# Optimization experiments

Measured on AMD Instinct MI355X. Metric: run time of the kernel, lower is better.

The kernel has to match this reference:

```python
import jax, jax.numpy as jnp
import numpy as np
from jax import lax

B, HCH, NCODES, H, W = 16, 32, 256, 256, 256

def conv2d(x, w, b, pad):
    y = lax.conv_general_dilated(x, w, (1, 1), [(pad, pad), (pad, pad)],
                                 dimension_numbers=('NCHW', 'OIHW', 'NCHW'))
    return y + b[None, :, None, None]

def vq(z, codebook):
    # z: (B,C,H,W); codebook: (K,C)
    zf = jnp.transpose(z, (0, 2, 3, 1)).reshape(-1, z.shape[1])  # (BHW,C)
    dists = (zf ** 2).sum(1, keepdims=True) + (codebook ** 2).sum(1) - 2.0 * zf @ codebook.T
    idx = jnp.argmin(dists, axis=1)
    zq = codebook[idx].reshape(z.shape[0], z.shape[2], z.shape[3], z.shape[1])
    zq = jnp.transpose(zq, (0, 3, 1, 2))
    # straight-through estimator
    return z + lax.stop_gradient(zq - z)

def setup_inputs() -> dict:
    key = jax.random.key(0)
    ks = jax.random.split(key, 12)
    s = lambda k, shp, scale=0.1: (jax.random.normal(k, shp, jnp.float32) * scale)
    return {
        'x': jax.random.normal(ks[0], (B, 1, H, W), jnp.float32),
        'stem_w': s(ks[1], (HCH, 1, 3, 3)),
        'stem_b': s(ks[2], (HCH,)),
        'up1_w': s(ks[3], (HCH, HCH, 3, 3)),
        'up1_b': s(ks[4], (HCH,)),
        'up2_w': s(ks[5], (HCH, HCH, 1, 1)),
        'up2_b': s(ks[6], (HCH,)),
        'tau_w': s(ks[7], (HCH, HCH, 1, 1)),
        'tau_b': s(ks[8], (HCH,)),
        'codebook': jax.random.uniform(ks[9], (NCODES, HCH), jnp.float32,
                                       -1.0 / NCODES, 1.0 / NCODES),
        'dec_w': s(ks[10], (1, HCH, 1, 1)),
        'dec_b': s(ks[11], (1,)),
        'n_steps': 5,
    }

def reference(x, stem_w, stem_b, up1_w, up1_b, up2_w, up2_b, tau_w, tau_b,
              codebook, dec_w, dec_b, n_steps):
    state = jax.nn.relu(conv2d(x, stem_w, stem_b, 1))
    for t in range(n_steps):
        delta = conv2d(jax.nn.relu(conv2d(state, up1_w, up1_b, 1)), up2_w, up2_b, 0)
        beta = jax.nn.sigmoid(conv2d(state, tau_w, tau_b, 0))
        state = beta * state + (1.0 - beta) * delta
        state = vq(state, codebook)  # vq_every = 1
    return jax.nn.sigmoid(conv2d(state, dec_w, dec_b, 0))
```

## Files before the change

### kernel.cpp

```cpp
#include <hip/hip_runtime.h>
#include <hip/hip_bf16.h>

#define BATCH 16
#define HH 256
#define WW 256
#define NPIX (BATCH*HH*WW)
#define NSTEPS 5
#define CBS 40

#define W1F 0
#define W2F 9216
#define WTF 10240
#define CBF 11264
#define IDF 19456
#define W1P 20480
#define W2P 29696
#define WTP 30720
#define IDP 31744
#define CBP 32768
#define FRAGS_TOT 40960

using u16 = unsigned short;
using u32 = unsigned int;
using u8  = unsigned char;

typedef __attribute__((ext_vector_type(8))) short bf8_t;
typedef __attribute__((ext_vector_type(4))) float f4_t;

#define MFMA16 __builtin_amdgcn_mfma_f32_16x16x32_bf16

#define DPPMIN(v, CTRL) do { \
    u32 _o = (u32)__builtin_amdgcn_update_dpp((int)(v), (int)(v), (CTRL), 0xF, 0xF, false); \
    (v) = _o < (v) ? _o : (v); } while (0)

#define LDS_ORDER() asm volatile("" ::: "memory")

__device__ __forceinline__ float bf2f(u32 u) {
    union { u32 i; float f; } v; v.i = u << 16; return v.f;
}
__device__ __forceinline__ u16 f2bf(float f) {
    union { float f; u32 i; } v; v.f = f;
    u32 x = v.i;
    x += 0x7fffu + ((x >> 16) & 1u);
    return (u16)(x >> 16);
}
__device__ __forceinline__ u32 pack2bf(float a, float b) {
    __hip_bfloat162 h2 = __float22bfloat162_rn(float2{a, b});
    union { __hip_bfloat162 h; u32 u; } v; v.h = h2; return v.u;
}
__device__ __forceinline__ float ldin(const void* p, int i, int f32) {
    return f32 ? ((const float*)p)[i] : bf2f(((const u16*)p)[i]);
}
__device__ __forceinline__ u16 ldbf(const void* p, int i, int f32) {
    return f32 ? f2bf(((const float*)p)[i]) : ((const u16*)p)[i];
}
__device__ __forceinline__ int sniff_f32(const void* xraw) {
    const u32* xw = (const u32*)xraw;
    int cnt = 0;
    for (int j = 0; j < 64; j++) {
        u32 w = xw[j];
        float flo = bf2f(w & 0xffffu);
        float a = fabsf(flo);
        if (flo == 0.0f || (a >= 6e-8f && a <= 64.0f)) cnt++;
    }
    return (cnt < 32) ? 1 : 0;
}
__device__ __forceinline__ int chperm(int kp) { return (kp >> 1) | ((kp & 1) << 4); }

__global__ void prep_kernel(const void* x,
    const void* stem_w, const void* stem_b, const void* up1_w, const void* up1_b,
    const void* up2_w, const void* up2_b, const void* tau_w, const void* tau_b,
    const void* cb, const void* dec_w, const void* dec_b,
    u16* frags, u16* cb_bf,
    float* cn2, float* cadj, float* decdot, float* wf0,
    float* up1_bf, float* up2_bf, float* tau_bf, float* stem_bf, int* flag)
{
    int f32 = sniff_f32(x);
    int i = blockIdx.x * 256 + threadIdx.x;
    if (i == 0) *flag = f32;
    if (i < 9216) {
        int slot = i >> 9, rem = i & 511, lane = rem >> 3, j = rem & 7;
        int tap = slot >> 1, nt = slot & 1;
        int co = nt*16 + (lane & 15), ci = (lane >> 4)*8 + j;
        frags[W1F + i] = ldbf(up1_w, (co*32+ci)*9 + tap, f32);
        return;
    }
    i -= 9216;
    if (i < 1024) {
        int nt = i >> 9, rem = i & 511, lane = rem >> 3, j = rem & 7;
        int co = nt*16 + (lane & 15), k = (lane >> 4)*8 + j;
        frags[W2F + i] = ldbf(up2_w, co*32 + k, f32);
        return;
    }
    i -= 1024;
    if (i < 1024) {
        int nt = i >> 9, rem = i & 511, lane = rem >> 3, j = rem & 7;
        int co = nt*16 + (lane & 15), k = (lane >> 4)*8 + j;
        frags[WTF + i] = ldbf(tau_w, co*32 + k, f32);
        return;
    }
    i -= 1024;
    if (i < 8192) {
        int nt = i >> 9, rem = i & 511, lane = rem >> 3, j = rem & 7;
        int code = nt*16 + (lane & 15), c = (lane >> 4)*8 + j;
        frags[CBF + i] = ldbf(cb, code*32 + c, f32);
        return;
    }
    i -= 8192;
    if (i < 1024) {
        int s = i >> 9, rem = i & 511, lane = rem >> 3, j = rem & 7;
        int colq = lane & 15, quad = lane >> 4;
        frags[IDF + i] = ((quad*8 + j) == (colq + s*16)) ? (u16)0x3F80 : (u16)0;
        return;
    }
    i -= 1024;
    if (i < 9216) {
        int slot = i >> 9, rem = i & 511, lane = rem >> 3, j = rem & 7;
        int tap = slot >> 1, nt = slot & 1;
        int co = nt*16 + (lane & 15), ci = chperm((lane >> 4)*8 + j);
        frags[W1P + i] = ldbf(up1_w, (co*32+ci)*9 + tap, f32);
        return;
    }
    i -= 9216;
    if (i < 1024) {
        int nt = i >> 9, rem = i & 511, lane = rem >> 3, j = rem & 7;
        int co = nt*16 + (lane & 15), k = chperm((lane >> 4)*8 + j);
        frags[W2P + i] = ldbf(up2_w, co*32 + k, f32);
        return;
    }
    i -= 1024;
    if (i < 1024) {
        int nt = i >> 9, rem = i & 511, lane = rem >> 3, j = rem & 7;
        int co = nt*16 + (lane & 15), k = chperm((lane >> 4)*8 + j);
        frags[WTP + i] = ldbf(tau_w, co*32 + k, f32);
        return;
    }
    i -= 1024;
    if (i < 1024) {
        int s = i >> 9, rem = i & 511, lane = rem >> 3, j = rem & 7;
        int colq = lane & 15, quad = lane >> 4;
        int ch = chperm(quad*8 + j);
        frags[IDP + i] = (ch == (colq + s*16)) ? (u16)0x3F80 : (u16)0;
        return;
    }
    i -= 1024;
    if (i < 8192) {
        int nt = i >> 9, rem = i & 511, lane = rem >> 3, j = rem & 7;
        int code = nt*16 + (lane & 15), c = chperm((lane >> 4)*8 + j);
        frags[CBP + i] = ldbf(cb, code*32 + c, f32);
        return;
    }
    i -= 8192;
    if (i < 257*CBS) {
        int row = i / CBS, p = i - row*CBS;
        cb_bf[i] = (p < 32 && row < 256) ? ldbf(cb, row*32 + chperm(p), f32) : (u16)0;
        return;
    }
    i -= 257*CBS;
    if (i < 256) {
        float s = 0.f;
        for (int c = 0; c < 32; c++) { float v = ldin(cb, i*32+c, f32); s += v*v; }
        cn2[i] = 0.5f * s;
        return;
    }
    i -= 256;
    if (i < 256) {
        float s = 0.f;
        for (int c = 0; c < 32; c++) { float v = ldin(cb, i*32+c, f32); s += v*v; }
        cadj[i] = 0.25f * (0.5f * s) + 0.5f;
        return;
    }
    i -= 256;
    if (i < 256) {
        float s = ldin(dec_b, 0, f32);
        for (int c = 0; c < 32; c++) s += ldin(dec_w, c, f32) * ldin(cb, i*32+c, f32);
        decdot[i] = s;
        return;
    }
    i -= 256;
    if (i < 288) {
        int tap = i >> 5, co = i & 31;
        wf0[i] = ldin(stem_w, co*9 + tap, f32);
        return;
    }
    i -= 288;
    if (i < 32) { up1_bf[i]  = ldin(up1_b, i, f32); return; }
    i -= 32;
    if (i < 32) { up2_bf[i]  = ldin(up2_b, i, f32); return; }
    i -= 32;
    if (i < 32) { tau_bf[i]  = ldin(tau_b, i, f32); return; }
    i -= 32;
    if (i < 32) { stem_bf[i] = ldin(stem_b, i, f32); return; }
}

__global__ __launch_bounds__(256) void step0_kernel(
    const void* __restrict__ xraw, const int* __restrict__ flagp,
    u8* __restrict__ idx_out,
    const u16* __restrict__ fragsg, const float* __restrict__ cn2,
    const float* __restrict__ up1_b, const float* __restrict__ up2_b,
    const float* __restrict__ tau_b, const float* __restrict__ wf0,
    const float* __restrict__ stem_bf)
{
    __shared__ __align__(16) u16 smem[31872];
    u16* w1f   = smem;
    u16* w2f   = smem + 9216;
    u16* wtf   = smem + 10240;
    u16* cbf   = smem + 11264;
    u16* tileq = smem + 19456;
    u16* hzb   = smem + 29824;
    float* xs  = (float*)hzb;

    int tid = threadIdx.x;
    int lane = tid & 63, wave = tid >> 6;
    int col = lane & 15, quad = lane >> 4;
    int b = blockIdx.z, x0 = blockIdx.x * 16, y0 = blockIdx.y * 16;

    {
        const uint4* s4 = (const uint4*)fragsg;
        uint4* d4 = (uint4*)smem;
        for (int i = tid; i < 2432; i += 256) d4[i] = s4[i];
    }

    {
        int f32 = *flagp;
        for (int pp = tid; pp < 400; pp += 256) {
            int r = pp / 20, c = pp - r*20;
            int gy = y0 - 2 + r, gx = x0 - 2 + c;
            float v = 0.f;
            if ((unsigned)gy < 256u && (unsigned)gx < 256u)
                v = ldin(xraw, (b << 16) | (gy << 8) | gx, f32);
            xs[pp] = v;
        }
        __syncthreads();
        for (int pp = tid; pp < 324; pp += 256) {
            int r = pp / 18, c = pp - r*18;
            int gy = y0 - 1 + r, gx = x0 - 1 + c;
            uint4 qv[4] = {{0,0,0,0},{0,0,0,0},{0,0,0,0},{0,0,0,0}};
            if ((unsigned)gy < 256u && (unsigned)gx < 256u) {
                float acc[32];
#pragma unroll
                for (int co = 0; co < 32; co++) acc[co] = stem_bf[co];
#pragma unroll
                for (int tap = 0; tap < 9; tap++) {
                    float v = xs[(r + tap/3)*20 + (c + tap%3)];
                    const float* w = &wf0[tap*32];
#pragma unroll
                    for (int co = 0; co < 32; co++) acc[co] = fmaf(v, w[co], acc[co]);
                }
                u32* ow = (u32*)qv;
#pragma unroll
                for (int j = 0; j < 16; j++)
                    ow[j] = pack2bf(fmaxf(acc[2*j], 0.f), fmaxf(acc[2*j+1], 0.f));
            }
#pragma unroll
            for (int q = 0; q < 4; q++)
                *(uint4*)&tileq[(q*324 + pp)*8] = qv[q];
        }
        __syncthreads();
    }
    __syncthreads();

    float cn2adj[16];
#pragma unroll
    for (int nt = 0; nt < 16; nt++) cn2adj[nt] = 0.25f*cn2[nt*16+col] + 0.5f;
    float bu1C0 = up1_b[col], bu1C1 = up1_b[col+16];
    float bu2_0 = up2_b[col], bu2_1 = up2_b[col+16];
    float bt0 = tau_b[col],   bt1 = tau_b[col+16];
    int qk0 = col >> 3, e = col & 7;
    u16* hzw = &hzb[wave*512];
    int wy = wave * 4;
    f4_t kz = {0.f,0.f,0.f,0.f};

    bf8_t rows[4][3];
#pragma unroll
    for (int i = 0; i < 4; i++)
#pragma unroll
        for (int dx = 0; dx < 3; dx++)
            rows[i][dx] = *(const bf8_t*)&tileq[(quad*324 + (wy+i)*18 + col+dx)*8];

#pragma unroll
    for (int rrp = 0; rrp < 2; rrp++) {
        if (rrp) {
#pragma unroll
            for (int dx = 0; dx < 3; dx++) {
                rows[0][dx] = rows[2][dx];
                rows[1][dx] = rows[3][dx];
                rows[2][dx] = *(const bf8_t*)&tileq[(quad*324 + (wy+4)*18 + col+dx)*8];
                rows[3][dx] = *(const bf8_t*)&tileq[(quad*324 + (wy+5)*18 + col+dx)*8];
            }
        }
        f4_t aA0 = kz, aA1 = kz, aB0 = kz, aB1 = kz;
#pragma unroll
        for (int t = 0; t < 9; t++) {
            int dy = t/3, dx = t - dy*3;
            bf8_t wA = *(const bf8_t*)&w1f[((t*2+0)*64 + lane)*8];
            bf8_t wB = *(const bf8_t*)&w1f[((t*2+1)*64 + lane)*8];
            aA0 = MFMA16(rows[dy  ][dx], wA, aA0, 0, 0, 0);
            aA1 = MFMA16(rows[dy  ][dx], wB, aA1, 0, 0, 0);
            aB0 = MFMA16(rows[dy+1][dx], wA, aB0, 0, 0, 0);
            aB1 = MFMA16(rows[dy+1][dx], wB, aB1, 0, 0, 0);
        }
#pragma unroll
        for (int r = 0; r < 4; r++) {
            int px = quad*4 + r;
            u32 pk = pack2bf(fmaxf(aA0[r] + bu1C0, 0.f), fmaxf(aA1[r] + bu1C1, 0.f));
            hzw[((qk0  )*16 + px)*8 + e] = (u16)pk;
            hzw[((qk0+2)*16 + px)*8 + e] = (u16)(pk >> 16);
        }
        asm volatile("s_waitcnt lgkmcnt(0)" ::: "memory");
        bf8_t hA0 = *(const bf8_t*)&hzw[(quad*16 + col)*8];
#pragma unroll
        for (int r = 0; r < 4; r++) {
            int px = quad*4 + r;
            u32 pk = pack2bf(fmaxf(aB0[r] + bu1C0, 0.f), fmaxf(aB1[r] + bu1C1, 0.f));
            hzw[((qk0  )*16 + px)*8 + e] = (u16)pk;
            hzw[((qk0+2)*16 + px)*8 + e] = (u16)(pk >> 16);
        }
        asm volatile("s_waitcnt lgkmcnt(0)" ::: "memory");
        bf8_t hA1 = *(const bf8_t*)&hzw[(quad*16 + col)*8];

        bf8_t w20 = *(const bf8_t*)&w2f[(0*64+lane)*8];
        bf8_t w21 = *(const bf8_t*)&w2f[(1*64+lane)*8];
        bf8_t wt0 = *(const bf8_t*)&wtf[(0*64+lane)*8];
        bf8_t wt1 = *(const bf8_t*)&wtf[(1*64+lane)*8];
        bf8_t sA0 = rows[1][1], sA1 = rows[2][1];
        f4_t d00 = MFMA16(hA0, w20, kz, 0, 0, 0);
        f4_t d01 = MFMA16(hA0, w21, kz, 0, 0, 0);
        f4_t d10 = MFMA16(hA1, w20, kz, 0, 0, 0);
        f4_t d11 = MFMA16(hA1, w21, kz, 0, 0, 0);
        f4_t t00 = MFMA16(sA0, wt0, kz, 0, 0, 0);
        f4_t t01 = MFMA16(sA0, wt1, kz, 0, 0, 0);
        f4_t t10 = MFMA16(sA1, wt0, kz, 0, 0, 0);
        f4_t t11 = MFMA16(sA1, wt1, kz, 0, 0, 0);

        int py0 = wy + rrp*2 + 1, py1 = py0 + 1;
#pragma unroll
        for (int r = 0; r < 4; r++) {
            int px = quad*4 + r, pxt = 1 + px;
            float s0 = bf2f(tileq[((col>>3    )*324 + py0*18 + pxt)*8 + (col&7)]);
            float s1 = bf2f(tileq[(((col>>3)+2)*324 + py0*18 + pxt)*8 + (col&7)]);
            float dl0 = d00[r] + bu2_0, tv0 = t00[r] + bt0;
            float be0 = 1.0f / (1.0f + __expf(-tv0));
            float dl1 = d01[r] + bu2_1, tv1 = t01[r] + bt1;
            float be1 = 1.0f / (1.0f + __expf(-tv1));
            u32 pk = pack2bf(-0.25f * (dl0 + be0*(s0 - dl0)),
                             -0.25f * (dl1 + be1*(s1 - dl1)));
            hzw[((qk0  )*16 + px)*8 + e] = (u16)pk;
            hzw[((qk0+2)*16 + px)*8 + e] = (u16)(pk >> 16);
        }
        asm volatile("s_waitcnt lgkmcnt(0)" ::: "memory");
        bf8_t zA0 = *(const bf8_t*)&hzw[(quad*16 + col)*8];
#pragma unroll
        for (int r = 0; r < 4; r++) {
            int px = quad*4 + r, pxt = 1 + px;
            float s0 = bf2f(tileq[((col>>3    )*324 + py1*18 + pxt)*8 + (col&7)]);
            float s1 = bf2f(tileq[(((col>>3)+2)*324 + py1*18 + pxt)*8 + (col&7)]);
            float dl0 = d10[r] + bu2_0, tv0 = t10[r] + bt0;
            float be0 = 1.0f / (1.0f + __expf(-tv0));
            float dl1 = d11[r] + bu2_1, tv1 = t11[r] + bt1;
            float be1 = 1.0f / (1.0f + __expf(-tv1));
            u32 pk = pack2bf(-0.25f * (dl0 + be0*(s0 - dl0)),
                             -0.25f * (dl1 + be1*(s1 - dl1)));
            hzw[((qk0  )*16 + px)*8 + e] = (u16)pk;
            hzw[((qk0+2)*16 + px)*8 + e] = (u16)(pk >> 16);
        }
        asm volatile("s_waitcnt lgkmcnt(0)" ::: "memory");
        bf8_t zA1 = *(const bf8_t*)&hzw[(quad*16 + col)*8];

        u32 b0[4], b1[4];
#pragma unroll
        for (int r = 0; r < 4; r++) { b0[r] = 0xFFFFFFFFu; b1[r] = 0xFFFFFFFFu; }
#pragma unroll
        for (int nt = 0; nt < 16; nt++) {
            bf8_t cf = *(const bf8_t*)&cbf[(nt*64 + lane)*8];
            f4_t ci = {cn2adj[nt], cn2adj[nt], cn2adj[nt], cn2adj[nt]};
            f4_t s0 = MFMA16(zA0, cf, ci, 0, 0, 0);
            f4_t s1 = MFMA16(zA1, cf, ci, 0, 0, 0);
            u32 code = (u32)(nt*16) | (u32)col;
#pragma unroll
            for (int r = 0; r < 4; r++) {
                u32 k0 = (__builtin_bit_cast(u32, s0[r]) & 0xFFFFFF00u) | code;
                u32 k1 = (__builtin_bit_cast(u32, s1[r]) & 0xFFFFFF00u) | code;
                b0[r] = k0 < b0[r] ? k0 : b0[r];
                b1[r] = k1 < b1[r] ? k1 : b1[r];
            }
        }
#pragma unroll
        for (int r = 0; r < 4; r++) {
            DPPMIN(b0[r], 0x121); DPPMIN(b0[r], 0x122);
            DPPMIN(b0[r], 0x124); DPPMIN(b0[r], 0x128);
            DPPMIN(b1[r], 0x121); DPPMIN(b1[r], 0x122);
            DPPMIN(b1[r], 0x124); DPPMIN(b1[r], 0x128);
        }
        int yr = y0 + wy + rrp*2;
        if (col < 4) {
            idx_out[(b*256 + yr    )*256 + x0 + quad*4 + col] = (u8)(b0[col] & 255u);
            idx_out[(b*256 + yr + 1)*256 + x0 + quad*4 + col] = (u8)(b1[col] & 255u);
        }
    }
}

__global__ __launch_bounds__(256) void step1_kernel(
    const u8* __restrict__ idx_in, u8* __restrict__ idx_out,
    const u16* __restrict__ fragsg, const u16* __restrict__ cbr_g,
    const float* __restrict__ cadj_g,
    const float* __restrict__ up1_b, const float* __restrict__ up2_b,
    const float* __restrict__ tau_b)
{
    __shared__ __align__(16) u16 smem[24104];
    u16* w1f = smem;
    u16* w2f = smem + 9216;
    u16* wtf = smem + 10240;
    u16* cbr = smem + 11264;
    float* cadjf = (float*)(smem + 21544);
    u16* hzb = smem + 22056;

    int tid = threadIdx.x;
    int lane = tid & 63, wave = tid >> 6;
    int col = lane & 15, quad = lane >> 4;
    int b = blockIdx.z, x0 = blockIdx.x * 16, y0 = blockIdx.y * 32;
    int wy = wave * 4;

    bf8_t id0 = *(const bf8_t*)&fragsg[IDP + (0*64+lane)*8];
    bf8_t id1 = *(const bf8_t*)&fragsg[IDP + (1*64+lane)*8];

    {
        const uint4* s4 = (const uint4*)(fragsg + W1P);
        uint4* d4 = (uint4*)smem;
        for (int i = tid; i < 1408; i += 256) d4[i] = s4[i];
        const uint4* c4 = (const uint4*)cbr_g;
        uint4* e4 = (uint4*)cbr;
        for (int i = tid; i < 1285; i += 256) e4[i] = c4[i];
        const uint4* a4 = (const uint4*)cadj_g;
        uint4* f4p = (uint4*)cadjf;
        if (tid < 64) f4p[tid] = a4[tid];
    }
    __syncthreads();

    float bu1C0 = up1_b[col], bu1C1 = up1_b[col+16];
    float bu2_0 = up2_b[col], bu2_1 = up2_b[col+16];
    float bt0 = tau_b[col],   bt1 = tau_b[col+16];
    u16* hzw = &hzb[wave*512];
    u32* hz32 = (u32*)hzw;
    f4_t kz = {0.f,0.f,0.f,0.f};

    for (int th = 0; th < 2; th++) {
        int yb = y0 + th*16;

        u32 kp[6];
#pragma unroll
        for (int tr = 0; tr < 6; tr++) {
            u32 pk = 0;
#pragma unroll
            for (int dx = 0; dx < 3; dx++) {
                int gy = yb - 1 + wy + tr, gx = x0 - 1 + col + dx;
                bool ok = ((unsigned)gy < 256u) & ((unsigned)gx < 256u);
                u32 c = ok ? (u32)idx_in[(b << 16) | (gy << 8) | gx] : 256u;
                pk |= c << (9*dx);
            }
            kp[tr] = pk;
        }

        f4_t acc[4][2];
#pragma unroll
        for (int r4 = 0; r4 < 4; r4++) { acc[r4][0] = kz; acc[r4][1] = kz; }
        bf8_t sA[4];
#pragma unroll
        for (int t = 0; t < 9; t++) {
            int dy = t/3, dx = t - dy*3;
            bf8_t wA = *(const bf8_t*)&w1f[((t*2+0)*64 + lane)*8];
            bf8_t wB = *(const bf8_t*)&w1f[((t*2+1)*64 + lane)*8];
#pragma unroll
            for (int r4 = 0; r4 < 4; r4++) {
                int k = (int)((kp[r4+dy] >> (9*dx)) & 511u);
                bf8_t f = *(const bf8_t*)&cbr[k*CBS + quad*8];
                if (t == 4) sA[r4] = f;
                acc[r4][0] = MFMA16(f, wA, acc[r4][0], 0, 0, 0);
                acc[r4][1] = MFMA16(f, wB, acc[r4][1], 0, 0, 0);
            }
        }

        bf8_t w20 = *(const bf8_t*)&w2f[(0*64+lane)*8];
        bf8_t w21 = *(const bf8_t*)&w2f[(1*64+lane)*8];
        bf8_t wt0 = *(const bf8_t*)&wtf[(0*64+lane)*8];
        bf8_t wt1 = *(const bf8_t*)&wtf[(1*64+lane)*8];

        bf8_t zA[4];
#pragma unroll
        for (int r4 = 0; r4 < 4; r4++) {
#pragma unroll
            for (int r = 0; r < 4; r++) {
                int px = quad*4 + r;
                hz32[px*16 + col] = pack2bf(fmaxf(acc[r4][0][r] + bu1C0, 0.f),
                                            fmaxf(acc[r4][1][r] + bu1C1, 0.f));
            }
            LDS_ORDER();
            bf8_t hA = *(const bf8_t*)&hzw[col*32 + quad*8];
            LDS_ORDER();
            f4_t d0 = MFMA16(hA, w20, kz, 0, 0, 0);
            f4_t d1 = MFMA16(hA, w21, kz, 0, 0, 0);
            f4_t t0 = MFMA16(sA[r4], wt0, kz, 0, 0, 0);
            f4_t t1 = MFMA16(sA[r4], wt1, kz, 0, 0, 0);
            f4_t Sl = MFMA16(sA[r4], id0, kz, 0, 0, 0);
            f4_t Sh = MFMA16(sA[r4], id1, kz, 0, 0, 0);
#pragma unroll
            for (int r = 0; r < 4; r++) {
                int px = quad*4 + r;
                float dl0 = d0[r] + bu2_0, tv0 = t0[r] + bt0;
                float be0 = 1.0f / (1.0f + __expf(-tv0));
                float dl1 = d1[r] + bu2_1, tv1 = t1[r] + bt1;
                float be1 = 1.0f / (1.0f + __expf(-tv1));
                hz32[px*16 + col] = pack2bf(-0.25f * (dl0 + be0*(Sl[r] - dl0)),
                                            -0.25f * (dl1 + be1*(Sh[r] - dl1)));
            }
            LDS_ORDER();
            zA[r4] = *(const bf8_t*)&hzw[col*32 + quad*8];
            LDS_ORDER();
        }

        u32 bk[4][4];
#pragma unroll
        for (int r4 = 0; r4 < 4; r4++)
#pragma unroll
            for (int r = 0; r < 4; r++) bk[r4][r] = 0xFFFFFFFFu;
#pragma unroll
        for (int nt = 0; nt < 16; nt++) {
            bf8_t cf = *(const bf8_t*)&cbr[(nt*16 + col)*CBS + quad*8];
            float ca = cadjf[nt*16 + col];
            f4_t ci = {ca, ca, ca, ca};
            u32 code = (u32)(nt*16) | (u32)col;
#pragma unroll
            for (int r4 = 0; r4 < 4; r4++) {
                f4_t sc = MFMA16(zA[r4], cf, ci, 0, 0, 0);
#pragma unroll
                for (int r = 0; r < 4; r++) {
                    u32 k0 = (__builtin_bit_cast(u32, sc[r]) & 0xFFFFFF00u) | code;
                    bk[r4][r] = k0 < bk[r4][r] ? k0 : bk[r4][r];
                }
            }
        }
#pragma unroll
        for (int r4 = 0; r4 < 4; r4++) {
#pragma unroll
            for (int r = 0; r < 4; r++) {
                DPPMIN(bk[r4][r], 0x121); DPPMIN(bk[r4][r], 0x122);
                DPPMIN(bk[r4][r], 0x124); DPPMIN(bk[r4][r], 0x128);
            }
            int yr = yb + wy + r4;
            if (col < 4)
                idx_out[(b*256 + yr)*256 + x0 + quad*4 + col] = (u8)(bk[r4][col] & 255u);
        }
    }
}

__global__ __launch_bounds__(256) void dec_kernel(const u8* __restrict__ idx,
        const float* __restrict__ decdot, const int* __restrict__ flagp,
        void* __restrict__ out)
{
    int p = blockIdx.x * 256 + threadIdx.x;
    float s = decdot[idx[p]];
    float r = 1.0f / (1.0f + __expf(-s));
    if (*flagp) ((float*)out)[p] = r;
    else        ((u16*)out)[p]   = f2bf(r);
}

extern "C" void kernel_launch(void* const* d_in, const int* in_sizes, int n_in,
                              void* d_out, int out_size, void* d_ws, size_t ws_size,
                              hipStream_t stream)
{
    const void* x      = d_in[0];
    const void* stem_w = d_in[1];
    const void* stem_b = d_in[2];
    const void* up1_w  = d_in[3];
    const void* up1_b  = d_in[4];
    const void* up2_w  = d_in[5];
    const void* up2_b  = d_in[6];
    const void* tau_w  = d_in[7];
    const void* tau_b  = d_in[8];
    const void* cb     = d_in[9];
    const void* dec_w  = d_in[10];
    const void* dec_b  = d_in[11];

    char* ws = (char*)d_ws;
    size_t off = 0;
    auto carve = [&](size_t bytes) -> void* {
        void* p = ws + off;
        off += (bytes + 255) & ~(size_t)255;
        return p;
    };
    u8*    idxA    = (u8*)   carve(NPIX);
    u8*    idxB    = (u8*)   carve(NPIX);
    u16*   frags   = (u16*)  carve(FRAGS_TOT * 2);
    u16*   cb_bf   = (u16*)  carve(257*CBS * 2);
    float* cn2     = (float*)carve(256 * 4);
    float* cadj    = (float*)carve(256 * 4);
    float* decdot  = (float*)carve(256 * 4);
    float* wf0     = (float*)carve(288 * 4);
    float* up1_bf  = (float*)carve(32 * 4);
    float* up2_bf  = (float*)carve(32 * 4);
    float* tau_bf  = (float*)carve(32 * 4);
    float* stem_bf = (float*)carve(32 * 4);
    int*   flag    = (int*)  carve(4);

    prep_kernel<<<205, 256, 0, stream>>>(x, stem_w, stem_b, up1_w, up1_b,
        up2_w, up2_b, tau_w, tau_b, cb, dec_w, dec_b,
        frags, cb_bf, cn2, cadj, decdot, wf0,
        up1_bf, up2_bf, tau_bf, stem_bf, flag);

    dim3 g0(WW/16, HH/16, BATCH);
    step0_kernel<<<g0, 256, 0, stream>>>(x, flag, idxA,
        frags, cn2, up1_bf, up2_bf, tau_bf, wf0, stem_bf);
    dim3 g1(WW/16, HH/32, BATCH);
    u8* cur = idxA; u8* nxt = idxB;
    for (int t = 1; t < NSTEPS; t++) {
        step1_kernel<<<g1, 256, 0, stream>>>(cur, nxt, frags, cb_bf, cadj,
                                             up1_bf, up2_bf, tau_bf);
        u8* tmp = cur; cur = nxt; nxt = tmp;
    }
    dec_kernel<<<NPIX/256, 256, 0, stream>>>(cur, decdot, flag, d_out);
}
```

Measured before the change: 458.6 us.

## Use identity MFMA for state transpose and packed u32 LDS scratch layout

Replaces the per-element bf16 scratch writes with single packed 32-bit stores in a pixel-major layout, so each lane writes one word instead of two halfwords. The centre-pixel state values are now produced with MFMAs against identity fragments instead of scalar LDS gathers from the tile. The stem output channel packing and the fragment copy are changed to match the new channel pairing (c, c+16). The identity fragments are loaded straight from global memory into registers, and one redundant barrier is dropped. This cuts LDS traffic and bank conflicts in the per-step epilogue at the cost of four extra MFMAs per row pair, and it depends on the new layout matching how the weight fragments are prepared.

Result: no change. 454.7 us (-0.8%).

```diff
diff --git a/kernel.cpp b/kernel.cpp
--- a/kernel.cpp
+++ b/kernel.cpp
@@ -215,10 +215,16 @@
     int col = lane & 15, quad = lane >> 4;
     int b = blockIdx.z, x0 = blockIdx.x * 16, y0 = blockIdx.y * 16;
 
+    bf8_t id0 = *(const bf8_t*)&fragsg[IDP + (0*64+lane)*8];
+    bf8_t id1 = *(const bf8_t*)&fragsg[IDP + (1*64+lane)*8];
+
     {
-        const uint4* s4 = (const uint4*)fragsg;
+        const uint4* s4 = (const uint4*)(fragsg + W1P);
         uint4* d4 = (uint4*)smem;
-        for (int i = tid; i < 2432; i += 256) d4[i] = s4[i];
+        for (int i = tid; i < 1408; i += 256) d4[i] = s4[i];
+        const uint4* c4 = (const uint4*)(fragsg + CBP);
+        uint4* e4 = (uint4*)cbf;
+        for (int i = tid; i < 1024; i += 256) e4[i] = c4[i];
     }
 
     {
@@ -249,14 +255,13 @@
                 }
                 u32* ow = (u32*)qv;
 #pragma unroll
-                for (int j = 0; j < 16; j++)
-                    ow[j] = pack2bf(fmaxf(acc[2*j], 0.f), fmaxf(acc[2*j+1], 0.f));
+                for (int m = 0; m < 16; m++)
+                    ow[m] = pack2bf(fmaxf(acc[m], 0.f), fmaxf(acc[m+16], 0.f));
             }
 #pragma unroll
             for (int q = 0; q < 4; q++)
                 *(uint4*)&tileq[(q*324 + pp)*8] = qv[q];
         }
-        __syncthreads();
     }
     __syncthreads();
 
@@ -266,8 +271,8 @@
     float bu1C0 = up1_b[col], bu1C1 = up1_b[col+16];
     float bu2_0 = up2_b[col], bu2_1 = up2_b[col+16];
     float bt0 = tau_b[col],   bt1 = tau_b[col+16];
-    int qk0 = col >> 3, e = col & 7;
     u16* hzw = &hzb[wave*512];
+    u32* hz32 = (u32*)hzw;
     int wy = wave * 4;
     f4_t kz = {0.f,0.f,0.f,0.f};
 
@@ -303,21 +308,21 @@
 #pragma unroll
         for (int r = 0; r < 4; r++) {
             int px = quad*4 + r;
-            u32 pk = pack2bf(fmaxf(aA0[r] + bu1C0, 0.f), fmaxf(aA1[r] + bu1C1, 0.f));
-            hzw[((qk0  )*16 + px)*8 + e] = (u16)pk;
-            hzw[((qk0+2)*16 + px)*8 + e] = (u16)(pk >> 16);
-        }
-        asm volatile("s_waitcnt lgkmcnt(0)" ::: "memory");
-        bf8_t hA0 = *(const bf8_t*)&hzw[(quad*16 + col)*8];
+            hz32[px*16 + col] = pack2bf(fmaxf(aA0[r] + bu1C0, 0.f),
+                                        fmaxf(aA1[r] + bu1C1, 0.f));
+        }
+        LDS_ORDER();
+        bf8_t hA0 = *(const bf8_t*)&hzw[col*32 + quad*8];
+        LDS_ORDER();
 #pragma unroll
         for (int r = 0; r < 4; r++) {
             int px = quad*4 + r;
-            u32 pk = pack2bf(fmaxf(aB0[r] + bu1C0, 0.f), fmaxf(aB1[r] + bu1C1, 0.f));
-            hzw[((qk0  )*16 + px)*8 + e] = (u16)pk;
-            hzw[((qk0+2)*16 + px)*8 + e] = (u16)(pk >> 16);
-        }
-        asm volatile("s_waitcnt lgkmcnt(0)" ::: "memory");
-        bf8_t hA1 = *(const bf8_t*)&hzw[(quad*16 + col)*8];
+            hz32[px*16 + col] = pack2bf(fmaxf(aB0[r] + bu1C0, 0.f),
+                                        fmaxf(aB1[r] + bu1C1, 0.f));
+        }
+        LDS_ORDER();
+        bf8_t hA1 = *(const bf8_t*)&hzw[col*32 + quad*8];
+        LDS_ORDER();
 
         bf8_t w20 = *(const bf8_t*)&w2f[(0*64+lane)*8];
         bf8_t w21 = *(const bf8_t*)&w2f[(1*64+lane)*8];
@@ -332,40 +337,37 @@
         f4_t t01 = MFMA16(sA0, wt1, kz, 0, 0, 0);
         f4_t t10 = MFMA16(sA1, wt0, kz, 0, 0, 0);
         f4_t t11 = MFMA16(sA1, wt1, kz, 0, 0, 0);
-
-        int py0 = wy + rrp*2 + 1, py1 = py0 + 1;
+        f4_t S0l = MFMA16(sA0, id0, kz, 0, 0, 0);
+        f4_t S0h = MFMA16(sA0, id1, kz, 0, 0, 0);
+        f4_t S1l = MFMA16(sA1, id0, kz, 0, 0, 0);
+        f4_t S1h = MFMA16(sA1, id1, kz, 0, 0, 0);
+
 #pragma unroll
         for (int r = 0; r < 4; r++) {
-            int px = quad*4 + r, pxt = 1 + px;
-            float s0 = bf2f(tileq[((col>>3    )*324 + py0*18 + pxt)*8 + (col&7)]);
-            float s1 = bf2f(tileq[(((col>>3)+2)*324 + py0*18 + pxt)*8 + (col&7)]);
+            int px = quad*4 + r;
             float dl0 = d00[r] + bu2_0, tv0 = t00[r] + bt0;
             float be0 = 1.0f / (1.0f + __expf(-tv0));
             float dl1 = d01[r] + bu2_1, tv1 = t01[r] + bt1;
             float be1 = 1.0f / (1.0f + __expf(-tv1));
-            u32 pk = pack2bf(-0.25f * (dl0 + be0*(s0 - dl0)),
-                             -0.25f * (dl1 + be1*(s1 - dl1)));
-            hzw[((qk0  )*16 + px)*8 + e] = (u16)pk;
-            hzw[((qk0+2)*16 + px)*8 + e] = (u16)(pk >> 16);
-        }
-        asm volatile("s_waitcnt lgkmcnt(0)" ::: "memory");
-        bf8_t zA0 = *(const bf8_t*)&hzw[(quad*16 + col)*8];
+            hz32[px*16 + col] = pack2bf(-0.25f * (dl0 + be0*(S0l[r] - dl0)),
+                                        -0.25f * (dl1 + be1*(S0h[r] - dl1)));
+        }
+        LDS_ORDER();
+        bf8_t zA0 = *(const bf8_t*)&hzw[col*32 + quad*8];
+        LDS_ORDER();
 #pragma unroll
         for (int r = 0; r < 4; r++) {
-            int px = quad*4 + r, pxt = 1 + px;
-            float s0 = bf2f(tileq[((col>>3    )*324 + py1*18 + pxt)*8 + (col&7)]);
-            float s1 = bf2f(tileq[(((col>>3)+2)*324 + py1*18 + pxt)*8 + (col&7)]);
+            int px = quad*4 + r;
             float dl0 = d10[r] + bu2_0, tv0 = t10[r] + bt0;
             float be0 = 1.0f / (1.0f + __expf(-tv0));
             float dl1 = d11[r] + bu2_1, tv1 = t11[r] + bt1;
             float be1 = 1.0f / (1.0f + __expf(-tv1));
-            u32 pk = pack2bf(-0.25f * (dl0 + be0*(s0 - dl0)),
-                             -0.25f * (dl1 + be1*(s1 - dl1)));
-            hzw[((qk0  )*16 + px)*8 + e] = (u16)pk;
-            hzw[((qk0+2)*16 + px)*8 + e] = (u16)(pk >> 16);
-        }
-        asm volatile("s_waitcnt lgkmcnt(0)" ::: "memory");
-        bf8_t zA1 = *(const bf8_t*)&hzw[(quad*16 + col)*8];
+            hz32[px*16 + col] = pack2bf(-0.25f * (dl0 + be0*(S1l[r] - dl0)),
+                                        -0.25f * (dl1 + be1*(S1h[r] - dl1)));
+        }
+        LDS_ORDER();
+        bf8_t zA1 = *(const bf8_t*)&hzw[col*32 + quad*8];
+        LDS_ORDER();
 
         u32 b0[4], b1[4];
 #pragma unroll
```
